# Performance work log

Hardware: AMD Instinct MI355X
Metric: run time of the kernel (lower is better)

## Reference

```python
import jax, jax.numpy as jnp
import numpy as np

D_MODEL = 1024
N_HEADS = 16
SEQ = 2048
BATCH = 2


def setup_inputs() -> dict:
    key = jax.random.key(0)
    ks = jax.random.split(key, 12)
    s = 1.0 / np.sqrt(D_MODEL)
    return {
        "q_input": jax.random.normal(ks[0], (BATCH, SEQ, D_MODEL), jnp.float32),
        "k_input": jax.random.normal(ks[1], (BATCH, SEQ, D_MODEL), jnp.float32),
        "v_input": jax.random.normal(ks[2], (BATCH, SEQ, D_MODEL), jnp.float32),
        "key_padding_mask": jnp.zeros((BATCH, SEQ), dtype=bool),
        "wq": jax.random.normal(ks[3], (D_MODEL, D_MODEL), jnp.float32) * s,
        "bq": jnp.zeros((D_MODEL,), jnp.float32),
        "wk": jax.random.normal(ks[4], (D_MODEL, D_MODEL), jnp.float32) * s,
        "bk": jnp.zeros((D_MODEL,), jnp.float32),
        "wv": jax.random.normal(ks[5], (D_MODEL, D_MODEL), jnp.float32) * s,
        "bv": jnp.zeros((D_MODEL,), jnp.float32),
        "wo": jax.random.normal(ks[6], (D_MODEL, D_MODEL), jnp.float32) * s,
        "bo": jnp.zeros((D_MODEL,), jnp.float32),
    }


def reference(q_input, k_input, v_input, key_padding_mask, wq, bq, wk, bk, wv, bv, wo, bo):
    B, Lq, _ = q_input.shape
    Lk = k_input.shape[1]
    d_head = D_MODEL // N_HEADS
    # torch Linear: x @ W.T + b
    Q = q_input @ wq.T + bq
    K = k_input @ wk.T + bk
    V = v_input @ wv.T + bv
    # [B, H, L, d_head]
    Qh = Q.reshape(B, Lq, N_HEADS, d_head).transpose(0, 2, 1, 3)
    Kh = K.reshape(B, Lk, N_HEADS, d_head).transpose(0, 2, 1, 3)
    Vh = V.reshape(B, Lk, N_HEADS, d_head).transpose(0, 2, 1, 3)
    scores = jnp.einsum("bhqd,bhkd->bhqk", Qh, Kh) / jnp.sqrt(jnp.float32(d_head))
    # causal mask (use_mask=True)
    causal = jnp.arange(Lk)[None, :] > jnp.arange(Lq)[:, None]  # [Lq, Lk]
    scores = jnp.where(causal[None, None], -jnp.inf, scores)
    # key padding mask [B,1,1,Lk]
    scores = jnp.where(key_padding_mask[:, None, None, :], -jnp.inf, scores)
    # module's global all-inf fallback (scalar condition)
    probs = jnp.where(
        jnp.all(jnp.isinf(scores)),
        jnp.full_like(scores, 1.0 / Lk),
        jax.nn.softmax(scores, axis=-1),
    )
    # dropout is identity in eval mode
    out = jnp.einsum("bhqk,bhkd->bhqd", probs, Vh)
    out = out.transpose(0, 2, 1, 3).reshape(B, Lq, D_MODEL)
    return out @ wo.T + bo
```

## Files before the change

kernel.cpp:

```cpp
#include <hip/hip_runtime.h>
#include <cstdint>
#include <cstddef>

#define DM   1024
#define HEADS 16
#define DH    64
#define SEQL  2048
#define BATCH 2
#define MTOT  (BATCH*SEQL)

typedef __attribute__((ext_vector_type(8))) short short8;
typedef __attribute__((ext_vector_type(4))) float floatx4;

__device__ __forceinline__ unsigned short f2bf(float f) {
  unsigned int u = __float_as_uint(f);
  u = (u + 0x7FFFu + ((u >> 16) & 1u)) >> 16;
  return (unsigned short)u;
}

__device__ __forceinline__ float exp2_fast(float x) {
#if __has_builtin(__builtin_amdgcn_exp2f)
  return __builtin_amdgcn_exp2f(x);
#else
  return exp2f(x);
#endif
}

__device__ __forceinline__ unsigned int cvt_pk_bf16(float lo, float hi) {
  unsigned int r;
  asm("v_cvt_pk_bf16_f32 %0, %1, %2" : "=v"(r) : "v"(lo), "v"(hi));
  return r;
}

__device__ __forceinline__ void async_ld16(const void* g, void* l) {
  __builtin_amdgcn_global_load_lds(
      (const __attribute__((address_space(1))) unsigned int*)g,
      (__attribute__((address_space(3))) unsigned int*)l, 16, 0, 0);
}

#define QSCALE 0.1803368801111204f

__global__ void cvt_w(const float* __restrict__ w0, const float* __restrict__ w1,
                      const float* __restrict__ w2, const float* __restrict__ w3,
                      unsigned short* __restrict__ W0, unsigned short* __restrict__ W1,
                      unsigned short* __restrict__ W2, unsigned short* __restrict__ W3) {
  const int bid = blockIdx.x;
  const int seg = bid >> 10;
  const int base = (bid & 1023) * 1024;
  const float* src = seg == 0 ? w0 : seg == 1 ? w1 : seg == 2 ? w2 : w3;
  unsigned short* dst = seg == 0 ? W0 : seg == 1 ? W1 : seg == 2 ? W2 : W3;
  int i = base + threadIdx.x * 4;
  float4 vv = *(const float4*)(src + i);
  ushort4 o;
  o.x = f2bf(vv.x); o.y = f2bf(vv.y); o.z = f2bf(vv.z); o.w = f2bf(vv.w);
  *(ushort4*)(dst + i) = o;
}

__global__ __launch_bounds__(256, 3) void qkv_gemm(
    const float* Xq, const float* Xk, const float* Xv,
    const unsigned short* Wq, const unsigned short* Wk, const unsigned short* Wv,
    const float* bq, const float* bk, const float* bv,
    unsigned short* Qo, unsigned short* Ko, unsigned short* VTo) {
  __shared__ unsigned short As[128 * 64], Bs[128 * 64];
  const float* A; const unsigned short* Bw; const float* bias; unsigned short* Cout;
  if (blockIdx.z == 0)      { A = Xq; Bw = Wq; bias = bq; Cout = Qo; }
  else if (blockIdx.z == 1) { A = Xk; Bw = Wk; bias = bk; Cout = Ko; }
  else                      { A = Xv; Bw = Wv; bias = bv; Cout = VTo; }

  const int K = DM, N = DM;
  const int m0 = blockIdx.y * 128, n0 = blockIdx.x * 128;
  const int tid  = threadIdx.x;
  const int lane = tid & 63, wvi = tid >> 6;
  const int lq = lane & 15, quad = lane >> 4;
  const int wrow = wvi >> 1, wcol = wvi & 1;

  floatx4 acc[4][4];
  #pragma unroll
  for (int i = 0; i < 4; i++)
    #pragma unroll
    for (int j = 0; j < 4; j++)
      #pragma unroll
      for (int e = 0; e < 4; e++) acc[i][j][e] = 0.0f;

  for (int kt = 0; kt < K; kt += 64) {
    #pragma unroll
    for (int cc = 0; cc < 4; cc++) {
      int c = wvi + cc * 4;
      int e = c * 512 + lane * 8;
      int r = e >> 6, col = e & 63;
      async_ld16(Bw + (size_t)(n0 + r) * K + kt + col, Bs + c * 512);
    }
    #pragma unroll
    for (int cc = 0; cc < 4; cc++) {
      int c = wvi + cc * 4;
      int e = c * 512 + lane * 8;
      int r = e >> 6, col = e & 63;
      const float* src = A + (size_t)(m0 + r) * K + kt + col;
      float4 f0 = *(const float4*)(src);
      float4 f1 = *(const float4*)(src + 4);
      uint4 w;
      w.x = cvt_pk_bf16(f0.x, f0.y);
      w.y = cvt_pk_bf16(f0.z, f0.w);
      w.z = cvt_pk_bf16(f1.x, f1.y);
      w.w = cvt_pk_bf16(f1.z, f1.w);
      *(uint4*)(As + c * 512 + lane * 8) = w;
    }
    __syncthreads();
    #pragma unroll
    for (int ks = 0; ks < 64; ks += 32) {
      short8 af[4], bf[4];
      #pragma unroll
      for (int i = 0; i < 4; i++)
        af[i] = *(const short8*)&As[(wrow * 64 + i * 16 + lq) * 64 + ks + quad * 8];
      #pragma unroll
      for (int j = 0; j < 4; j++)
        bf[j] = *(const short8*)&Bs[(wcol * 64 + j * 16 + lq) * 64 + ks + quad * 8];
      #pragma unroll
      for (int i = 0; i < 4; i++)
        #pragma unroll
        for (int j = 0; j < 4; j++)
          acc[i][j] = __builtin_amdgcn_mfma_f32_16x16x32_bf16(af[i], bf[j], acc[i][j], 0, 0, 0);
    }
    __syncthreads();
  }

  if (blockIdx.z == 2) {
    #pragma unroll
    for (int i = 0; i < 4; i++) {
      const int rowg = m0 + wrow * 64 + i * 16 + quad * 4;
      const int bb  = rowg >> 11;
      const int kt2 = (rowg & 2047) >> 6;
      const int k0  = rowg & 63;
      #pragma unroll
      for (int j = 0; j < 4; j++) {
        const int colg = n0 + wcol * 64 + j * 16 + lq;
        const int h2 = colg >> 6, d2 = colg & 63;
        const float bb_v = bias[colg];
        ushort4 w;
        w.x = f2bf(acc[i][j][0] + bb_v);
        w.y = f2bf(acc[i][j][1] + bb_v);
        w.z = f2bf(acc[i][j][2] + bb_v);
        w.w = f2bf(acc[i][j][3] + bb_v);
        *(ushort4*)(Cout + (size_t)((bb * HEADS + h2) * 32 + kt2) * 4096 + d2 * 64 + k0) = w;
      }
    }
  } else {
    const float oscale = (blockIdx.z == 0) ? QSCALE : 1.0f;
    #pragma unroll
    for (int i = 0; i < 4; i++) {
      #pragma unroll
      for (int j = 0; j < 4; j++) {
        int colg = n0 + wcol * 64 + j * 16 + lq;
        float bb = bias[colg];
        #pragma unroll
        for (int r = 0; r < 4; r++) {
          int rowg = m0 + wrow * 64 + i * 16 + quad * 4 + r;
          Cout[(size_t)rowg * N + colg] = f2bf((acc[i][j][r] + bb) * oscale);
        }
      }
    }
  }
}

__global__ __launch_bounds__(256, 4) void out_gemm(
    const unsigned short* __restrict__ A, const unsigned short* __restrict__ Bw,
    const float* __restrict__ bias, float* __restrict__ C) {
  __shared__ unsigned short As[64 * 64], Bs[128 * 64];
  const int K = DM, N = DM;
  const int m0 = blockIdx.y * 64, n0 = blockIdx.x * 128;
  const int tid  = threadIdx.x;
  const int lane = tid & 63, wvi = tid >> 6;
  const int lq = lane & 15, quad = lane >> 4;

  floatx4 acc[8];
  #pragma unroll
  for (int j = 0; j < 8; j++)
    #pragma unroll
    for (int e = 0; e < 4; e++) acc[j][e] = 0.0f;

  for (int kt = 0; kt < K; kt += 64) {
    #pragma unroll
    for (int cc = 0; cc < 2; cc++) {
      int c = wvi + cc * 4;
      int e = c * 512 + lane * 8;
      int r = e >> 6, col = e & 63;
      async_ld16(A + (size_t)(m0 + r) * K + kt + col, As + c * 512);
    }
    #pragma unroll
    for (int cc = 0; cc < 4; cc++) {
      int c = wvi + cc * 4;
      int e = c * 512 + lane * 8;
      int r = e >> 6, col = e & 63;
      async_ld16(Bw + (size_t)(n0 + r) * K + kt + col, Bs + c * 512);
    }
    __syncthreads();
    #pragma unroll
    for (int ks = 0; ks < 64; ks += 32) {
      const short8 af = *(const short8*)&As[(wvi * 16 + lq) * 64 + ks + quad * 8];
      #pragma unroll
      for (int j = 0; j < 8; j++) {
        const short8 bf = *(const short8*)&Bs[(j * 16 + lq) * 64 + ks + quad * 8];
        acc[j] = __builtin_amdgcn_mfma_f32_16x16x32_bf16(af, bf, acc[j], 0, 0, 0);
      }
    }
    __syncthreads();
  }

  #pragma unroll
  for (int j = 0; j < 8; j++) {
    const int colg = n0 + j * 16 + lq;
    const float bb = bias[colg];
    #pragma unroll
    for (int r = 0; r < 4; r++) {
      const int rowg = m0 + wvi * 16 + quad * 4 + r;
      C[(size_t)rowg * N + colg] = acc[j][r] + bb;
    }
  }
}

__global__ __launch_bounds__(256, 4) void attn_kernel(
    const unsigned short* __restrict__ Q, const unsigned short* __restrict__ K,
    const unsigned short* __restrict__ VT, const unsigned char* __restrict__ kpm,
    unsigned short* __restrict__ O) {
  __shared__ unsigned short Ks[64 * 72];
  __shared__ unsigned short VTs[64 * 72];
  __shared__ unsigned short Ps[4][16 * 72];

  const int bid = blockIdx.x;
  const int qt = 31 - (bid >> 5);
  const int bh = bid & 31;
  const int h = bh & 15, b = bh >> 4;
  const int tid = threadIdx.x, lane = tid & 63, wvi = tid >> 6;
  const int lq = lane & 15, quad = lane >> 4;
  const size_t bbase = (size_t)b * SEQL * DM;

  const int srow = tid >> 4;
  const int scol = (tid & 15) * 4;

  const unsigned short* kptr = K + bbase + (size_t)h * DH + (size_t)srow * DM + scol;
  const unsigned short* vptr = VT + (size_t)(b * HEADS + h) * 32 * 4096 + srow * 64 + scol;
  const unsigned char*  mptr = kpm + (size_t)b * SEQL + quad * 4;

  const unsigned short* Qrow = Q + bbase + (size_t)(qt * 64 + wvi * 16 + lq) * DM + h * DH;
  const short8 qf0 = *(const short8*)(Qrow + quad * 8);
  const short8 qf1 = *(const short8*)(Qrow + 32 + quad * 8);

  ushort4 kr[4], vr[4];
  unsigned int mr[4];
  #pragma unroll
  for (int j = 0; j < 4; j++) {
    kr[j] = *(const ushort4*)(kptr + (size_t)j * 16 * DM);
    vr[j] = *(const ushort4*)(vptr + j * 1024);
  }
  #pragma unroll
  for (int t = 0; t < 4; t++) mr[t] = *(const unsigned int*)(mptr + t * 16);
  kptr += (size_t)64 * DM; vptr += 4096; mptr += 64;

  floatx4 o[4];
  #pragma unroll
  for (int t = 0; t < 4; t++)
    #pragma unroll
    for (int e = 0; e < 4; e++) o[t][e] = 0.f;

  floatx4 lacc;
  #pragma unroll
  for (int e = 0; e < 4; e++) lacc[e] = 0.f;

  floatx4 zf;
  #pragma unroll
  for (int e = 0; e < 4; e++) zf[e] = 0.f;

  short8 ones8;
  #pragma unroll
  for (int e = 0; e < 8; e++) ones8[e] = (short)0x3F80;

  const int qg = wvi * 16 + lq;

  auto tile_body = [&](bool diag, const unsigned int* mcur) {
    floatx4 st[4];
    __builtin_amdgcn_s_setprio(1);
    #pragma unroll
    for (int t = 0; t < 4; t++) {
      const short8 a0 = *(const short8*)&Ks[(t * 16 + lq) * 72 + quad * 8];
      const short8 a1 = *(const short8*)&Ks[(t * 16 + lq) * 72 + 32 + quad * 8];
      st[t] = __builtin_amdgcn_mfma_f32_16x16x32_bf16(a0, qf0, zf, 0, 0, 0);
      st[t] = __builtin_amdgcn_mfma_f32_16x16x32_bf16(a1, qf1, st[t], 0, 0, 0);
    }
    __builtin_amdgcn_s_setprio(0);

    float x[4][4];
    #pragma unroll
    for (int t = 0; t < 4; t++)
      #pragma unroll
      for (int r = 0; r < 4; r++) x[t][r] = st[t][r];

    if (__any((int)((mcur[0] | mcur[1] | mcur[2] | mcur[3]) != 0u))) {
      #pragma unroll
      for (int t = 0; t < 4; t++)
        #pragma unroll
        for (int r = 0; r < 4; r++)
          if ((mcur[t] >> (8 * r)) & 0xffu) x[t][r] = -1e33f;
    }
    if (diag) {
      #pragma unroll
      for (int t = 0; t < 4; t++)
        #pragma unroll
        for (int r = 0; r < 4; r++)
          if (t * 16 + quad * 4 + r > qg) x[t][r] = -1e33f;
    }

    #pragma unroll
    for (int t = 0; t < 4; t++)
      #pragma unroll
      for (int r = 0; r < 4; r++)
        x[t][r] = exp2_fast(x[t][r]);

    #pragma unroll
    for (int t = 0; t < 4; t++) {
      unsigned int p01 = cvt_pk_bf16(x[t][0], x[t][1]);
      unsigned int p23 = cvt_pk_bf16(x[t][2], x[t][3]);
      *(uint2*)&Ps[wvi][lq * 72 + t * 16 + quad * 4] = make_uint2(p01, p23);
    }

    const short8 pa0 = *(const short8*)&Ps[wvi][lq * 72 + quad * 8];
    const short8 pa1 = *(const short8*)&Ps[wvi][lq * 72 + 32 + quad * 8];
    __builtin_amdgcn_s_setprio(1);
    #pragma unroll
    for (int t = 0; t < 4; t++) {
      const short8 b0 = *(const short8*)&VTs[(t * 16 + lq) * 72 + quad * 8];
      const short8 b1 = *(const short8*)&VTs[(t * 16 + lq) * 72 + 32 + quad * 8];
      o[t] = __builtin_amdgcn_mfma_f32_16x16x32_bf16(pa0, b0, o[t], 0, 0, 0);
      o[t] = __builtin_amdgcn_mfma_f32_16x16x32_bf16(pa1, b1, o[t], 0, 0, 0);
    }
    lacc = __builtin_amdgcn_mfma_f32_16x16x32_bf16(pa0, ones8, lacc, 0, 0, 0);
    lacc = __builtin_amdgcn_mfma_f32_16x16x32_bf16(pa1, ones8, lacc, 0, 0, 0);
    __builtin_amdgcn_s_setprio(0);
  };

  for (int kt = 0; kt < qt; kt++) {
    __syncthreads();
    #pragma unroll
    for (int j = 0; j < 4; j++) {
      *(ushort4*)&Ks [(j * 16 + srow) * 72 + scol] = kr[j];
      *(ushort4*)&VTs[(j * 16 + srow) * 72 + scol] = vr[j];
    }
    unsigned int mcur[4];
    #pragma unroll
    for (int t = 0; t < 4; t++) mcur[t] = mr[t];
    __syncthreads();

    #pragma unroll
    for (int j = 0; j < 4; j++) {
      kr[j] = *(const ushort4*)(kptr + (size_t)j * 16 * DM);
      vr[j] = *(const ushort4*)(vptr + j * 1024);
    }
    #pragma unroll
    for (int t = 0; t < 4; t++) mr[t] = *(const unsigned int*)(mptr + t * 16);
    kptr += (size_t)64 * DM; vptr += 4096; mptr += 64;

    tile_body(false, mcur);
  }

  __syncthreads();
  #pragma unroll
  for (int j = 0; j < 4; j++) {
    *(ushort4*)&Ks [(j * 16 + srow) * 72 + scol] = kr[j];
    *(ushort4*)&VTs[(j * 16 + srow) * 72 + scol] = vr[j];
  }
  __syncthreads();
  tile_body(true, mr);

  float linv[4];
  #pragma unroll
  for (int r = 0; r < 4; r++) linv[r] = 1.0f / lacc[r];
  #pragma unroll
  for (int t = 0; t < 4; t++)
    #pragma unroll
    for (int r = 0; r < 4; r++) {
      const int rowg = qt * 64 + wvi * 16 + quad * 4 + r;
      const int colg = h * 64 + t * 16 + lq;
      O[bbase + (size_t)rowg * DM + colg] = f2bf(o[t][r] * linv[r]);
    }
}

extern "C" void kernel_launch(void* const* d_in, const int* in_sizes, int n_in,
                              void* d_out, int out_size, void* d_ws, size_t ws_size,
                              hipStream_t stream) {
  const float* qin = (const float*)d_in[0];
  const float* kin = (const float*)d_in[1];
  const float* vin = (const float*)d_in[2];
  const unsigned char* kpm = (const unsigned char*)d_in[3];
  const float* wq = (const float*)d_in[4];
  const float* bq = (const float*)d_in[5];
  const float* wk = (const float*)d_in[6];
  const float* bk = (const float*)d_in[7];
  const float* wv = (const float*)d_in[8];
  const float* bv = (const float*)d_in[9];
  const float* wo = (const float*)d_in[10];
  const float* bo = (const float*)d_in[11];

  const size_t XN = (size_t)MTOT * DM;
  const size_t WN = (size_t)DM * DM;
  unsigned short* Wqb = (unsigned short*)d_ws;
  unsigned short* Wkb = Wqb + WN;
  unsigned short* Wvb = Wkb + WN;
  unsigned short* Wob = Wvb + WN;
  unsigned short* Qb  = Wob + WN;
  unsigned short* Kb  = Qb  + XN;
  unsigned short* VTg = Kb  + XN;
  unsigned short* Ob  = VTg + XN;

  cvt_w<<<dim3(4096), 256, 0, stream>>>(wq, wk, wv, wo, Wqb, Wkb, Wvb, Wob);

  dim3 g1(DM / 128, MTOT / 128, 3);
  qkv_gemm<<<g1, 256, 0, stream>>>(qin, kin, vin, Wqb, Wkb, Wvb, bq, bk, bv, Qb, Kb, VTg);

  attn_kernel<<<dim3(BATCH * HEADS * (SEQL / 64)), 256, 0, stream>>>(Qb, Kb, VTg, kpm, Ob);

  dim3 g2(DM / 128, MTOT / 64, 1);
  out_gemm<<<g2, 256, 0, stream>>>(Ob, Wob, bo, (float*)d_out);
}
```

Baseline: 239.6 us.

## Prefetch fp32 A tiles into registers and remap QKV blocks per XCD

The QKV projection GEMM now loads the next 64-wide K slice of fp32 activations into registers while the current slice is converted and fed to MFMA, double-buffering the global A loads across K steps. The 3D grid is flattened to 768 blocks and remapped so that all eight N-blocks sharing an M panel land on the same XCD, which should improve L2 reuse of the activation rows. Restrict qualifiers are added to the inputs. The register prefetch doubles the live A registers (16 float4), which may pressure occupancy under launch_bounds(256,3).

```diff
diff --git a/kernel.cpp b/kernel.cpp
--- a/kernel.cpp
+++ b/kernel.cpp
@@ -57,18 +57,29 @@
 }
 
 __global__ __launch_bounds__(256, 3) void qkv_gemm(
-    const float* Xq, const float* Xk, const float* Xv,
-    const unsigned short* Wq, const unsigned short* Wk, const unsigned short* Wv,
-    const float* bq, const float* bk, const float* bv,
+    const float* __restrict__ Xq, const float* __restrict__ Xk, const float* __restrict__ Xv,
+    const unsigned short* __restrict__ Wq, const unsigned short* __restrict__ Wk,
+    const unsigned short* __restrict__ Wv,
+    const float* __restrict__ bq, const float* __restrict__ bk, const float* __restrict__ bv,
     unsigned short* Qo, unsigned short* Ko, unsigned short* VTo) {
   __shared__ unsigned short As[128 * 64], Bs[128 * 64];
+
+  const int bid  = blockIdx.x;
+  const int xcd  = bid & 7;
+  const int idx  = bid >> 3;
+  const int pgrp = idx >> 3;
+  const int nblk = idx & 7;
+  const int panel = xcd + 8 * pgrp;
+  const int mblk = panel & 31;
+  const int z    = panel >> 5;
+
   const float* A; const unsigned short* Bw; const float* bias; unsigned short* Cout;
-  if (blockIdx.z == 0)      { A = Xq; Bw = Wq; bias = bq; Cout = Qo; }
-  else if (blockIdx.z == 1) { A = Xk; Bw = Wk; bias = bk; Cout = Ko; }
-  else                      { A = Xv; Bw = Wv; bias = bv; Cout = VTo; }
+  if (z == 0)      { A = Xq; Bw = Wq; bias = bq; Cout = Qo; }
+  else if (z == 1) { A = Xk; Bw = Wk; bias = bk; Cout = Ko; }
+  else             { A = Xv; Bw = Wv; bias = bv; Cout = VTo; }
 
   const int K = DM, N = DM;
-  const int m0 = blockIdx.y * 128, n0 = blockIdx.x * 128;
+  const int m0 = mblk * 128, n0 = nblk * 128;
   const int tid  = threadIdx.x;
   const int lane = tid & 63, wvi = tid >> 6;
   const int lq = lane & 15, quad = lane >> 4;
@@ -82,27 +93,36 @@
       #pragma unroll
       for (int e = 0; e < 4; e++) acc[i][j][e] = 0.0f;
 
-  for (int kt = 0; kt < K; kt += 64) {
+  float4 aregA[8], aregB[8];
+
+  auto loadA = [&](float4 (&r)[8], int kt) {
     #pragma unroll
     for (int cc = 0; cc < 4; cc++) {
       int c = wvi + cc * 4;
       int e = c * 512 + lane * 8;
-      int r = e >> 6, col = e & 63;
-      async_ld16(Bw + (size_t)(n0 + r) * K + kt + col, Bs + c * 512);
-    }
+      int rr = e >> 6, col = e & 63;
+      const float* src = A + (size_t)(m0 + rr) * K + kt + col;
+      r[cc * 2]     = *(const float4*)(src);
+      r[cc * 2 + 1] = *(const float4*)(src + 4);
+    }
+  };
+
+  auto step = [&](float4 (&r)[8], int kt) {
     #pragma unroll
     for (int cc = 0; cc < 4; cc++) {
       int c = wvi + cc * 4;
       int e = c * 512 + lane * 8;
-      int r = e >> 6, col = e & 63;
-      const float* src = A + (size_t)(m0 + r) * K + kt + col;
-      float4 f0 = *(const float4*)(src);
-      float4 f1 = *(const float4*)(src + 4);
+      int rr = e >> 6, col = e & 63;
+      async_ld16(Bw + (size_t)(n0 + rr) * K + kt + col, Bs + c * 512);
+    }
+    #pragma unroll
+    for (int cc = 0; cc < 4; cc++) {
+      int c = wvi + cc * 4;
       uint4 w;
-      w.x = cvt_pk_bf16(f0.x, f0.y);
-      w.y = cvt_pk_bf16(f0.z, f0.w);
-      w.z = cvt_pk_bf16(f1.x, f1.y);
-      w.w = cvt_pk_bf16(f1.z, f1.w);
+      w.x = cvt_pk_bf16(r[cc * 2].x,     r[cc * 2].y);
+      w.y = cvt_pk_bf16(r[cc * 2].z,     r[cc * 2].w);
+      w.z = cvt_pk_bf16(r[cc * 2 + 1].x, r[cc * 2 + 1].y);
+      w.w = cvt_pk_bf16(r[cc * 2 + 1].z, r[cc * 2 + 1].w);
       *(uint4*)(As + c * 512 + lane * 8) = w;
     }
     __syncthreads();
@@ -122,9 +142,17 @@
           acc[i][j] = __builtin_amdgcn_mfma_f32_16x16x32_bf16(af[i], bf[j], acc[i][j], 0, 0, 0);
     }
     __syncthreads();
-  }
-
-  if (blockIdx.z == 2) {
+  };
+
+  loadA(aregA, 0);
+  for (int kt = 0; kt < K; kt += 128) {
+    loadA(aregB, kt + 64);
+    step(aregA, kt);
+    if (kt + 128 < K) loadA(aregA, kt + 128);
+    step(aregB, kt + 64);
+  }
+
+  if (z == 2) {
     #pragma unroll
     for (int i = 0; i < 4; i++) {
       const int rowg = m0 + wrow * 64 + i * 16 + quad * 4;
@@ -145,7 +173,7 @@
       }
     }
   } else {
-    const float oscale = (blockIdx.z == 0) ? QSCALE : 1.0f;
+    const float oscale = (z == 0) ? QSCALE : 1.0f;
     #pragma unroll
     for (int i = 0; i < 4; i++) {
       #pragma unroll
@@ -412,8 +440,7 @@
 
   cvt_w<<<dim3(4096), 256, 0, stream>>>(wq, wk, wv, wo, Wqb, Wkb, Wvb, Wob);
 
-  dim3 g1(DM / 128, MTOT / 128, 3);
-  qkv_gemm<<<g1, 256, 0, stream>>>(qin, kin, vin, Wqb, Wkb, Wvb, bq, bk, bv, Qb, Kb, VTg);
+  qkv_gemm<<<dim3(768), 256, 0, stream>>>(qin, kin, vin, Wqb, Wkb, Wvb, bq, bk, bv, Qb, Kb, VTg);
 
   attn_kernel<<<dim3(BATCH * HEADS * (SEQL / 64)), 256, 0, stream>>>(Qb, Kb, VTg, kpm, Ob);
 
```

Measured after the change: 330.7 us. 38.0% more time.
